# Performance work log

Measured on AMD Instinct MI355X. Metric: run time of the kernel, lower is better.

## Reference

```python
import jax, jax.numpy as jnp
import numpy as np

KERNEL_NUM = 21
SIGMA = 0.1
EXACT_SIGMA = 0.001

def _kernel_params(k=KERNEL_NUM, sigma=SIGMA, exact_sigma=EXACT_SIGMA):
    step = 1.0 / (k - 1)
    left = -1.0 + step
    right = 1.0 - step
    mu = np.hstack([np.arange(left, right, (right - left) / (k - 2)), right, 1.0])
    sig = np.where(mu == 1.0, exact_sigma, sigma)
    return jnp.asarray(mu, jnp.float32), jnp.asarray(sig, jnp.float32)

MU, SIG = _kernel_params()

def setup_inputs() -> dict:
    key = jax.random.key(0)
    ks = jax.random.split(key, 11)
    B, LQ, LD, V, E = 1024, 20, 200, 100000, 128
    return {
        "q1": jax.random.randint(ks[0], (B, LQ), 0, V),
        "d1": jax.random.randint(ks[1], (B, LD), 0, V),
        "q2": jax.random.randint(ks[2], (B, LQ), 0, V),
        "d2": jax.random.randint(ks[3], (B, LD), 0, V),
        "emb": jax.random.normal(ks[4], (V, E), jnp.float32),
        "W1": jax.random.normal(ks[5], (10, 21), jnp.float32) * 0.1,
        "b1": jax.random.normal(ks[6], (10,), jnp.float32) * 0.1,
        "W2": jax.random.normal(ks[7], (5, 10), jnp.float32) * 0.1,
        "b2": jax.random.normal(ks[8], (5,), jnp.float32) * 0.1,
        "W3": jax.random.normal(ks[9], (1, 5), jnp.float32) * 0.1,
        "b3": jax.random.normal(ks[10], (1,), jnp.float32) * 0.1,
    }

def _matching_matrix(emb, q_ids, d_ids, alpha=1e-6):
    q = emb[q_ids]  # [B,LQ,E]
    d = emb[d_ids]  # [B,LD,E]
    nom = jnp.einsum('bqe,bde->bqd', q, d)
    qn = jnp.sqrt(jnp.sum(q * q, axis=2) + alpha)  # [B,LQ]
    dn = jnp.sqrt(jnp.sum(d * d, axis=2) + alpha)  # [B,LD]
    return nom / (qn[:, :, None] * dn[:, None, :])  # [B,LQ,LD]

def _apply_kernels(M):
    # M: [B,LQ,LD] -> phi: [B,LQ,LD,K]
    phi = jnp.exp(-jnp.square(M[..., None] - MU) / (2.0 * SIG * SIG))
    return jnp.sum(jnp.log1p(jnp.sum(phi, axis=2)), axis=1)  # [B,K]

def _mlp(x, W1, b1, W2, b2, W3, b3):
    x = jax.nn.relu(x)
    x = x @ W1.T + b1
    x = jax.nn.relu(x)
    x = x @ W2.T + b2
    x = jax.nn.relu(x)
    return x @ W3.T + b3  # [B,1]

def _predict(emb, q, d, W1, b1, W2, b2, W3, b3):
    M = _matching_matrix(emb, q, d)
    k = _apply_kernels(M)
    return _mlp(k, W1, b1, W2, b2, W3, b3)

def reference(q1, d1, q2, d2, emb, W1, b1, W2, b2, W3, b3):
    l1 = _predict(emb, q1, d1, W1, b1, W2, b2, W3, b3)
    l2 = _predict(emb, q2, d2, W1, b1, W2, b2, W3, b3)
    return jax.nn.sigmoid(l1 - l2)  # [B,1]
```

## Files before the change

### kernel.cpp

```cpp
#include <hip/hip_runtime.h>

#define NB 1024
#define LQ 20
#define LD 200
#define E4 32
#define NK 21
#define NTILE 13

typedef __attribute__((ext_vector_type(8))) short bf16x8;
typedef __attribute__((ext_vector_type(4))) float f32x4;

__device__ __forceinline__ short f2bf(float f, float& back) {
    unsigned u = __builtin_bit_cast(unsigned, f);
    unsigned r = (u + 0x7FFFu + ((u >> 16) & 1u)) >> 16;
    back = __builtin_bit_cast(float, r << 16);
    return (short)r;
}

__device__ __forceinline__ bf16x8 make_frag(float4 f0, float4 f1, float& sq) {
    bf16x8 v; float bk;
    v[0] = f2bf(f0.x, bk); sq += bk * bk;
    v[1] = f2bf(f0.y, bk); sq += bk * bk;
    v[2] = f2bf(f0.z, bk); sq += bk * bk;
    v[3] = f2bf(f0.w, bk); sq += bk * bk;
    v[4] = f2bf(f1.x, bk); sq += bk * bk;
    v[5] = f2bf(f1.y, bk); sq += bk * bk;
    v[6] = f2bf(f1.z, bk); sq += bk * bk;
    v[7] = f2bf(f1.w, bk); sq += bk * bk;
    return v;
}

__device__ __forceinline__ float fast_exp2(float x) {
#if __has_builtin(__builtin_amdgcn_exp2f)
    return __builtin_amdgcn_exp2f(x);
#else
    return __expf(x * 0.69314718056f);
#endif
}

__device__ __forceinline__ void rbf_accum(float m, float* S) {
    const float CK[20] = {
        2.52616e-20f, 2.04697e-16f, 6.10193e-13f, 6.69158e-10f, 2.69958e-7f,
        4.00653e-5f,  2.18749e-3f,  4.39369e-2f,  3.24652e-1f,  8.82497e-1f,
        8.82497e-1f,  3.24652e-1f,  4.39369e-2f,  2.18749e-3f,  4.00653e-5f,
        2.69958e-7f,  6.69158e-10f, 6.10193e-13f, 2.04697e-16f, 2.52616e-20f };
    const float a  = -72.13475204f * m * m;
    const float bb = 144.26950408f * m;
    #pragma unroll
    for (int k = 0; k < 20; ++k) {
        const float mu = 0.1f * (float)k - 0.95f;
        S[k] = fmaf(CK[k], fast_exp2(fmaf(bb, mu, a)), S[k]);
    }
    const float d = m - 1.0f;
    S[20] += fast_exp2(-721347.5204f * d * d);
}

__global__ __launch_bounds__(256, 3) void knrm_main(
    const int* __restrict__ q1, const int* __restrict__ d1,
    const int* __restrict__ q2, const int* __restrict__ d2,
    const float* __restrict__ emb,
    const float* __restrict__ W1, const float* __restrict__ b1,
    const float* __restrict__ W2, const float* __restrict__ b2,
    const float* __restrict__ W3, const float* __restrict__ b3,
    float* __restrict__ logits)
{
    __shared__ float sPhiW[4][LQ][NK];
    __shared__ float sX[NK];
    __shared__ float sH1[10];
    __shared__ float sH2[5];

    const int bp   = blockIdx.x;
    const int b    = bp & (NB - 1);
    const int pred = bp >> 10;
    const int t    = threadIdx.x;
    const int lane = t & 63, wave = t >> 6;
    const int c    = lane & 15, quad = lane >> 4;
    const int* __restrict__ qi = pred ? q2 : q1;
    const int* __restrict__ di = pred ? d2 : d1;
    const float4* emb4 = (const float4*)emb;

    int qid[2];
    #pragma unroll
    for (int Mt = 0; Mt < 2; ++Mt) {
        int row = Mt * 16 + c; row = row < LQ ? row : LQ - 1;
        qid[Mt] = qi[b * LQ + row];
    }
    int idv[4];
    #pragma unroll
    for (int tt = 0; tt < 4; ++tt) {
        int j = (wave + tt * 4) * 16 + c; j = j < LD ? j : LD - 1;
        idv[tt] = di[b * LD + j];
    }

    bf16x8 aF[2][4];
    float rqA = 0.f, rqB = 0.f;
    #pragma unroll
    for (int Mt = 0; Mt < 2; ++Mt) {
        const float4* qb = emb4 + (size_t)(unsigned)qid[Mt] * E4;
        float qs = 0.f;
        #pragma unroll
        for (int ks = 0; ks < 4; ++ks) {
            float4 f0 = qb[ks * 8 + quad * 2];
            float4 f1 = qb[ks * 8 + quad * 2 + 1];
            aF[Mt][ks] = make_frag(f0, f1, qs);
        }
        if (Mt == 1 && c >= LQ - 16) {
            #pragma unroll
            for (int ks = 0; ks < 4; ++ks) aF[Mt][ks] = (bf16x8)0;
            qs = 0.f;
        }
        qs += __shfl_xor(qs, 16);
        qs += __shfl_xor(qs, 32);
        const float rq = rsqrtf(qs + 1e-6f);
        if (Mt == 0) rqA = rq; else rqB = rq;
    }

    float S0[NK], S1[NK];
    #pragma unroll
    for (int k = 0; k < NK; ++k) { S0[k] = 0.f; S1[k] = 0.f; }

    #pragma unroll
    for (int tt = 0; tt < 4; ++tt) {
        const int tile = wave + tt * 4;
        if (tile >= NTILE) break;

        const float4* db = emb4 + (size_t)(unsigned)idv[tt] * E4;
        bf16x8 bF[4];
        float dsq = 0.f;
        #pragma unroll
        for (int ks = 0; ks < 4; ++ks) {
            float4 f0 = db[ks * 8 + quad * 2];
            float4 f1 = db[ks * 8 + quad * 2 + 1];
            bF[ks] = make_frag(f0, f1, dsq);
        }
        if (tile * 16 + c >= LD) {
            #pragma unroll
            for (int ks = 0; ks < 4; ++ks) bF[ks] = (bf16x8)0;
            dsq = 0.f;
        }
        dsq += __shfl_xor(dsq, 16);
        dsq += __shfl_xor(dsq, 32);
        const float rdc = rsqrtf(dsq + 1e-6f);
        float rdv[4];
        #pragma unroll
        for (int r = 0; r < 4; ++r) rdv[r] = __shfl(rdc, quad * 4 + r);

        f32x4 acc0 = {0.f, 0.f, 0.f, 0.f};
        f32x4 acc1 = {0.f, 0.f, 0.f, 0.f};
        #pragma unroll
        for (int ks = 0; ks < 4; ++ks) {
            acc0 = __builtin_amdgcn_mfma_f32_16x16x32_bf16(bF[ks], aF[0][ks], acc0, 0, 0, 0);
            acc1 = __builtin_amdgcn_mfma_f32_16x16x32_bf16(bF[ks], aF[1][ks], acc1, 0, 0, 0);
        }

        #pragma unroll
        for (int r = 0; r < 4; ++r) {
            rbf_accum(acc0[r] * rdv[r] * rqA, S0);
            rbf_accum(acc1[r] * rdv[r] * rqB, S1);
        }
    }

    #pragma unroll
    for (int k = 0; k < NK; ++k) {
        S0[k] += __shfl_xor(S0[k], 16);
        S0[k] += __shfl_xor(S0[k], 32);
        S1[k] += __shfl_xor(S1[k], 16);
        S1[k] += __shfl_xor(S1[k], 32);
    }
    if (quad == 0) {
        #pragma unroll
        for (int k = 0; k < NK; ++k) sPhiW[wave][c][k] = S0[k];
    } else if (quad == 1 && c < LQ - 16) {
        #pragma unroll
        for (int k = 0; k < NK; ++k) sPhiW[wave][16 + c][k] = S1[k];
    }
    __syncthreads();

    if (t < NK) {
        const float mu_t = 0.1f * (float)t - 0.95f;
        const float pad  = (t < 20) ? 8.0f * fast_exp2(-72.13475204f * mu_t * mu_t) : 0.0f;
        float s = 0.f;
        #pragma unroll
        for (int i = 0; i < LQ; ++i) {
            const float v = sPhiW[0][i][t] + sPhiW[1][i][t]
                          + sPhiW[2][i][t] + sPhiW[3][i][t] - pad;
            s += __logf(1.0f + v);
        }
        sX[t] = fmaxf(s, 0.f);
    }
    __syncthreads();

    if (t < 10) {
        float v = b1[t];
        #pragma unroll
        for (int k = 0; k < NK; ++k) v += W1[t * NK + k] * sX[k];
        sH1[t] = fmaxf(v, 0.f);
    }
    __syncthreads();

    if (t < 5) {
        float v = b2[t];
        #pragma unroll
        for (int k = 0; k < 10; ++k) v += W2[t * 10 + k] * sH1[k];
        sH2[t] = fmaxf(v, 0.f);
    }
    __syncthreads();

    if (t == 0) {
        float v = b3[0];
        #pragma unroll
        for (int k = 0; k < 5; ++k) v += W3[k] * sH2[k];
        logits[pred * NB + b] = v;
    }
}

__global__ void knrm_combine(const float* __restrict__ logits, float* __restrict__ out)
{
    const int b = blockIdx.x * blockDim.x + threadIdx.x;
    if (b < NB) {
        out[b] = 1.0f / (1.0f + __expf(logits[NB + b] - logits[b]));
    }
}

extern "C" void kernel_launch(void* const* d_in, const int* in_sizes, int n_in,
                              void* d_out, int out_size, void* d_ws, size_t ws_size,
                              hipStream_t stream) {
    float* logits = (float*)d_ws;
    knrm_main<<<2 * NB, 256, 0, stream>>>(
        (const int*)d_in[0], (const int*)d_in[1],
        (const int*)d_in[2], (const int*)d_in[3],
        (const float*)d_in[4],
        (const float*)d_in[5], (const float*)d_in[6],
        (const float*)d_in[7], (const float*)d_in[8],
        (const float*)d_in[9], (const float*)d_in[10],
        logits);
    knrm_combine<<<(NB + 255) / 256, 256, 0, stream>>>(logits, (float*)d_out);
}
```

Baseline: 153.0 us.

## Replace per-kernel exp with geometric recurrence and compact padded second query tile

The RBF accumulation now computes one exp for the center kernel and two ratio exps, then derives the neighbouring Gaussian kernels by repeated multiplication, which cuts the transcendental count per matching value from 21 to 4. The second MFMA tile, where only 4 of 16 query rows are valid, is compacted with shuffles so each lane evaluates one useful value instead of four mostly padded ones. The final reduction gains two extra xor-shuffles and a new writeback mask to match the new lane mapping. The recurrence can lose accuracy or underflow for the far kernels.

```diff
diff --git a/kernel.cpp b/kernel.cpp
--- a/kernel.cpp
+++ b/kernel.cpp
@@ -39,17 +39,24 @@
 }
 
 __device__ __forceinline__ void rbf_accum(float m, float* S) {
-    const float CK[20] = {
-        2.52616e-20f, 2.04697e-16f, 6.10193e-13f, 6.69158e-10f, 2.69958e-7f,
-        4.00653e-5f,  2.18749e-3f,  4.39369e-2f,  3.24652e-1f,  8.82497e-1f,
-        8.82497e-1f,  3.24652e-1f,  4.39369e-2f,  2.18749e-3f,  4.00653e-5f,
-        2.69958e-7f,  6.69158e-10f, 6.10193e-13f, 2.04697e-16f, 2.52616e-20f };
-    const float a  = -72.13475204f * m * m;
-    const float bb = 144.26950408f * m;
-    #pragma unroll
-    for (int k = 0; k < 20; ++k) {
-        const float mu = 0.1f * (float)k - 0.95f;
-        S[k] = fmaf(CK[k], fast_exp2(fmaf(bb, mu, a)), S[k]);
+    const float x = m - 0.05f;
+    const float p = fast_exp2(-72.13475204f * x * x);
+    S[10] += p;
+    float u = fast_exp2(fmaf(m, 14.4269504089f, -1.44269504089f));
+    float q = p;
+    #pragma unroll
+    for (int k = 11; k <= 19; ++k) {
+        q *= u;
+        S[k] += q;
+        u *= 0.36787944117f;
+    }
+    float v = fast_exp2(m * -14.4269504089f);
+    q = p;
+    #pragma unroll
+    for (int k = 9; k >= 0; --k) {
+        q *= v;
+        S[k] += q;
+        v *= 0.36787944117f;
     }
     const float d = m - 1.0f;
     S[20] += fast_exp2(-721347.5204f * d * d);
@@ -154,25 +161,38 @@
         }
 
         #pragma unroll
-        for (int r = 0; r < 4; ++r) {
+        for (int r = 0; r < 4; ++r)
             rbf_accum(acc0[r] * rdv[r] * rqA, S0);
-            rbf_accum(acc1[r] * rdv[r] * rqB, S1);
-        }
+
+        float m1[4];
+        #pragma unroll
+        for (int r = 0; r < 4; ++r) m1[r] = acc1[r] * rdv[r] * rqB;
+        const int src = (lane & 48) | ((lane >> 2) & 3);
+        const float g0 = __shfl(m1[0], src);
+        const float g1 = __shfl(m1[1], src);
+        const float g2 = __shfl(m1[2], src);
+        const float g3 = __shfl(m1[3], src);
+        const int rsel = lane & 3;
+        const float mv = (rsel == 0) ? g0 : (rsel == 1) ? g1 : (rsel == 2) ? g2 : g3;
+        rbf_accum(mv, S1);
     }
 
     #pragma unroll
     for (int k = 0; k < NK; ++k) {
         S0[k] += __shfl_xor(S0[k], 16);
         S0[k] += __shfl_xor(S0[k], 32);
+        S1[k] += __shfl_xor(S1[k], 1);
+        S1[k] += __shfl_xor(S1[k], 2);
         S1[k] += __shfl_xor(S1[k], 16);
         S1[k] += __shfl_xor(S1[k], 32);
     }
     if (quad == 0) {
         #pragma unroll
         for (int k = 0; k < NK; ++k) sPhiW[wave][c][k] = S0[k];
-    } else if (quad == 1 && c < LQ - 16) {
-        #pragma unroll
-        for (int k = 0; k < NK; ++k) sPhiW[wave][16 + c][k] = S1[k];
+    }
+    if ((lane & 51) == 0) {
+        #pragma unroll
+        for (int k = 0; k < NK; ++k) sPhiW[wave][16 + (lane >> 2)][k] = S1[k];
     }
     __syncthreads();
 
```

New measurement: 148.3 us. 1.03x faster.
